# Kernel optimization log

Measured on AMD Instinct MI355X. Metric: run time of the kernel, lower is better.

## Reference

```python
import jax, jax.numpy as jnp
import numpy as np

B, S, H, V, MAXLEN = 32, 128, 512, 32000, 64


def setup_inputs() -> dict:
    key = jax.random.key(0)
    ks = jax.random.split(key, 10)
    s = 0.05
    return {
        "word_level_rep": jax.random.normal(ks[0], (B, S, H), jnp.float32),
        "sentence_level_rep": jax.random.normal(ks[1], (B, H), jnp.float32),
        "W2": jax.random.normal(ks[2], (H,), jnp.float32) * s,          # Linear(H,1,bias=False)
        "W4": jax.random.normal(ks[3], (H, 2 * H), jnp.float32) * s,    # Linear(2H,H,bias=False), torch layout [out,in]
        "W_ih": jax.random.normal(ks[4], (4 * H, H), jnp.float32) * s,  # LSTM gates i,f,g,o
        "W_hh": jax.random.normal(ks[5], (4 * H, H), jnp.float32) * s,
        "b_ih": jax.random.normal(ks[6], (4 * H,), jnp.float32) * s,
        "b_hh": jax.random.normal(ks[7], (4 * H,), jnp.float32) * s,
        "W_out": jax.random.normal(ks[8], (V, H), jnp.float32) * s,
        "b_out": jax.random.normal(ks[9], (V,), jnp.float32) * s,
        "max_len": MAXLEN,
    }


def reference(word_level_rep, sentence_level_rep, W2, W4, W_ih, W_hh, b_ih, b_hh, W_out, b_out, max_len):
    b, seq, h_dim = word_level_rep.shape

    def step(carry, _):
        h, c = carry
        # sentence-level attention over a singleton memory bank -> weight == 1
        sent_ctx = sentence_level_rep                                   # [B,H]
        # word-level Bahdanau attention
        scores = jnp.tanh(word_level_rep + h[:, None, :]) @ W2          # [B,S]
        attn = jax.nn.softmax(scores, axis=1)                           # [B,S]
        word_ctx = jnp.einsum('bs,bsh->bh', attn, word_level_rep)       # [B,H]
        x = jnp.tanh(jnp.concatenate([sent_ctx, word_ctx], axis=-1) @ W4.T)  # [B,H]
        # PyTorch LSTM cell: gates order i, f, g, o
        gates = x @ W_ih.T + b_ih + h @ W_hh.T + b_hh                   # [B,4H]
        i, f, g, o = jnp.split(gates, 4, axis=-1)
        c_new = jax.nn.sigmoid(f) * c + jax.nn.sigmoid(i) * jnp.tanh(g)
        h_new = jax.nn.sigmoid(o) * jnp.tanh(c_new)
        out = h_new @ W_out.T + b_out                                   # [B,V]
        return (h_new, c_new), out

    h0 = jnp.zeros((b, h_dim), word_level_rep.dtype)
    c0 = jnp.zeros((b, h_dim), word_level_rep.dtype)
    (h_fin, _), outs = jax.lax.scan(step, (h0, c0), None, length=max_len)
    generated_sequence = jnp.transpose(outs, (1, 0, 2))                 # [B,max_len,V]
    return generated_sequence, h_fin
```

## Files before the change

kernel.cpp:

```cpp
#include <hip/hip_runtime.h>
#include <stdint.h>

typedef unsigned short ushort_t;
typedef unsigned long long ull_t;
typedef __attribute__((ext_vector_type(8))) short bf16x8;
typedef __attribute__((ext_vector_type(8))) unsigned short u16x8;
typedef __attribute__((ext_vector_type(4))) unsigned short u16x4;
typedef __attribute__((ext_vector_type(4))) float f32x4;
typedef __attribute__((ext_vector_type(4))) unsigned u32x4;

#define DEV static __device__ __forceinline__
#define SCOPE_AGENT __HIP_MEMORY_SCOPE_AGENT

DEV unsigned short f2bf(float f) {
  unsigned u = __float_as_uint(f);
  u += 0x7FFFu + ((u >> 16) & 1u);
  return (unsigned short)(u >> 16);
}
DEV float bf2f(unsigned short h) { return __uint_as_float(((unsigned)h) << 16); }
DEV float fast_rcp(float x) { return __builtin_amdgcn_rcpf(x); }
DEV float fast_tanh(float x) { float e = __expf(2.f * x); return (e - 1.f) * fast_rcp(e + 1.f); }
DEV float fast_sigm(float x) { return fast_rcp(1.f + __expf(-x)); }

DEV float wave_sum(float v) {
#pragma unroll
  for (int d = 32; d > 0; d >>= 1) v += __shfl_xor(v, d, 64);
  return v;
}
DEV float wave_max(float v) {
#pragma unroll
  for (int d = 32; d > 0; d >>= 1) v = fmaxf(v, __shfl_xor(v, d, 64));
  return v;
}

DEV void async_g2l(const void* g, void* l) {
  __builtin_amdgcn_global_load_lds((const __attribute__((address_space(1))) void*)g,
                                   (__attribute__((address_space(3))) void*)l, 16, 0, 0);
}

DEV unsigned ld_flag(unsigned* p) { return __hip_atomic_load(p, __ATOMIC_RELAXED, SCOPE_AGENT); }
DEV void st_flag(unsigned* p, unsigned v) { __hip_atomic_store(p, v, __ATOMIC_RELAXED, SCOPE_AGENT); }
DEV void st_u64(ull_t* p, ull_t v) { __hip_atomic_store(p, v, __ATOMIC_RELAXED, SCOPE_AGENT); }
DEV void release_fence() { __builtin_amdgcn_s_waitcnt(0); }

DEV u32x4 ld_coh16(const void* p) {
  u32x4 v;
  asm volatile("global_load_dwordx4 %0, %1, off sc0 sc1" : "=v"(v) : "v"(p));
  return v;
}
DEV void wait_vm0() { asm volatile("s_waitcnt vmcnt(0)" ::: "memory"); }

__global__ __launch_bounds__(256) void k_initP(
    const float* __restrict__ w, const float* __restrict__ sent,
    const float* __restrict__ W4, ushort_t* __restrict__ P, float* __restrict__ sp)
{
  __shared__ float As2[16 * 68];
  __shared__ float Bs2[16 * 68];
  const int tid = threadIdx.x;
  const int m0 = blockIdx.x * 64, n0 = blockIdx.y * 64;
  const int tm = tid & 15, tn = tid >> 4;
  const bool sent_half = (m0 >= 4096);
  float acc[4][4];
#pragma unroll
  for (int i = 0; i < 4; i++)
#pragma unroll
    for (int j = 0; j < 4; j++) acc[i][j] = 0.f;

  for (int k0 = 0; k0 < 512; k0 += 16) {
#pragma unroll
    for (int i = 0; i < 4; i++) {
      int idx = i * 256 + tid;
      int r = idx >> 4, kk = idx & 15;
      int m = m0 + r;
      float va = 0.f;
      if (m < 4096) va = w[(size_t)m * 512 + k0 + kk];
      else if (m < 4128) va = sent[(m - 4096) * 512 + k0 + kk];
      As2[kk * 68 + r] = va;
      Bs2[kk * 68 + r] = W4[(size_t)(n0 + r) * 1024 + (sent_half ? 0 : 512) + k0 + kk];
    }
    __syncthreads();
#pragma unroll
    for (int k = 0; k < 16; k++) {
      f32x4 av = *(const f32x4*)&As2[k * 68 + tm * 4];
      f32x4 bv = *(const f32x4*)&Bs2[k * 68 + tn * 4];
#pragma unroll
      for (int i = 0; i < 4; i++)
#pragma unroll
        for (int j = 0; j < 4; j++) acc[i][j] = fmaf(av[i], bv[j], acc[i][j]);
    }
    __syncthreads();
  }
#pragma unroll
  for (int i = 0; i < 4; i++) {
    int m = m0 + tm * 4 + i;
    if (m >= 4128) continue;
#pragma unroll
    for (int j = 0; j < 4; j++) {
      int n = n0 + tn * 4 + j;
      if (m < 4096) P[(size_t)m * 512 + n] = f2bf(acc[i][j]);
      else sp[(m - 4096) * 512 + n] = acc[i][j];
    }
  }
}

struct GateS {
  ushort_t XH[32 * 520];
  float gates[32 * 132];
  float bias[128];
  float cstate[1024];
  ushort_t hs16[1024];
};
struct AttnS {
  float hs[512];
  float sps[512];
  float sc[128];
  float attw[128];
  float xpart[8 * 520];
  ushort_t xs16[512];
};

__global__ __launch_bounds__(512, 2) void k_recur(
    const float* __restrict__ W2, const float* __restrict__ W_ih, const float* __restrict__ W_hh,
    const float* __restrict__ b_ih, const float* __restrict__ b_hh,
    const float* __restrict__ word, const ushort_t* __restrict__ P, const float* __restrict__ sp,
    unsigned* hflag, unsigned* xflag, ull_t* hbuf, ull_t* xbuf,
    ull_t* __restrict__ h_A, float* __restrict__ h_fin,
    const float* __restrict__ W_out, ushort_t* __restrict__ Wout_bf)
{
  __shared__ union { GateS g; AttnS a; } sm;
  const int bid = blockIdx.x, tid = threadIdx.x;
  const int wv = tid >> 6, lane = tid & 63;

  if (bid >= 48) {
    int idx = (bid - 48) * 512 + tid;
    const int stp = (256 - 48) * 512;
    for (; idx < 4096000; idx += stp) {
      f32x4 v = *(const f32x4*)(W_out + (size_t)idx * 4);
      u16x4 o;
      o[0] = f2bf(v[0]); o[1] = f2bf(v[1]); o[2] = f2bf(v[2]); o[3] = f2bf(v[3]);
      *(u16x4*)(Wout_bf + (size_t)idx * 4) = o;
    }
    return;
  }

  if (bid < 16) {
    const int ln = lane & 15, quad = lane >> 4;
    const int grow = (wv >> 1) * 512 + (bid << 5) + ((wv & 1) << 4) + ln;
    sm.g.cstate[tid] = 0.f;
    sm.g.cstate[tid + 512] = 0.f;
    if (tid < 128) {
      int gr = (tid >> 5) * 512 + (bid << 5) + (tid & 31);
      sm.g.bias[tid] = b_ih[gr] + b_hh[gr];
    }
    bf16x8 fih[16], fhh[16];
#pragma unroll
    for (int ks = 0; ks < 16; ks++) {
      const float* pi = W_ih + (size_t)grow * 512 + ks * 32 + quad * 8;
      const float* ph = W_hh + (size_t)grow * 512 + ks * 32 + quad * 8;
#pragma unroll
      for (int j = 0; j < 8; j++) {
        fih[ks][j] = (short)f2bf(pi[j]);
        fhh[ks][j] = (short)f2bf(ph[j]);
      }
    }
    __syncthreads();

#define STAGE_XH(SRC)                                                         \
    {                                                                         \
      const char* src_ = (const char*)(SRC);                                  \
      u32x4 r0 = ld_coh16(src_ + (tid << 4));                                 \
      u32x4 r1 = ld_coh16(src_ + ((512 + tid) << 4));                         \
      u32x4 r2 = ld_coh16(src_ + ((1024 + tid) << 4));                        \
      u32x4 r3 = ld_coh16(src_ + ((1536 + tid) << 4));                        \
      wait_vm0();                                                             \
      int c1 = 512 + tid, c2 = 1024 + tid, c3 = 1536 + tid;                   \
      *(u32x4*)&sm.g.XH[(tid >> 6) * 520 + (tid & 63) * 8] = r0;              \
      *(u32x4*)&sm.g.XH[(c1 >> 6) * 520 + (c1 & 63) * 8] = r1;                \
      *(u32x4*)&sm.g.XH[(c2 >> 6) * 520 + (c2 & 63) * 8] = r2;                \
      *(u32x4*)&sm.g.XH[(c3 >> 6) * 520 + (c3 & 63) * 8] = r3;                \
    }

#define GATE_MFMA(FW)                                                         \
    _Pragma("unroll")                                                         \
    for (int ks = 0; ks < 16; ks++) {                                         \
      bf16x8 a0 = *(const bf16x8*)&sm.g.XH[ln * 520 + ks * 32 + quad * 8];    \
      bf16x8 a1 = *(const bf16x8*)&sm.g.XH[(16 + ln) * 520 + ks * 32 + quad * 8]; \
      acc0 = __builtin_amdgcn_mfma_f32_16x16x32_bf16(a0, FW[ks], acc0, 0, 0, 0);  \
      acc1 = __builtin_amdgcn_mfma_f32_16x16x32_bf16(a1, FW[ks], acc1, 0, 0, 0);  \
    }

    for (int t = 0; t < 64; t++) {
      if (t > 0 && tid < 16) {
        while (ld_flag(&hflag[tid]) < (unsigned)t) __builtin_amdgcn_s_sleep(1);
      }
      __syncthreads();
      STAGE_XH(hbuf + ((t + 1) & 1) * 4096);
      __syncthreads();
      f32x4 acc0 = {0.f, 0.f, 0.f, 0.f}, acc1 = {0.f, 0.f, 0.f, 0.f};
      GATE_MFMA(fhh)
      if (tid < 32) {
        while (ld_flag(&xflag[tid]) < (unsigned)(t + 1)) __builtin_amdgcn_s_sleep(1);
      }
      __syncthreads();
      STAGE_XH(xbuf);
      __syncthreads();
      GATE_MFMA(fih)
      {
        float bb = sm.g.bias[wv * 16 + ln];
#pragma unroll
        for (int reg = 0; reg < 4; reg++) {
          sm.g.gates[(quad * 4 + reg) * 132 + wv * 16 + ln] = acc0[reg] + bb;
          sm.g.gates[(16 + quad * 4 + reg) * 132 + wv * 16 + ln] = acc1[reg] + bb;
        }
      }
      __syncthreads();
#pragma unroll
      for (int i = 0; i < 2; i++) {
        int e = i * 512 + tid;
        int b = e >> 5, hd = e & 31;
        float gi = sm.g.gates[b * 132 + hd];
        float gf = sm.g.gates[b * 132 + 32 + hd];
        float gg = sm.g.gates[b * 132 + 64 + hd];
        float go = sm.g.gates[b * 132 + 96 + hd];
        float cold = sm.g.cstate[e];
        float cn = fast_sigm(gf) * cold + fast_sigm(gi) * fast_tanh(gg);
        float hn = fast_sigm(go) * fast_tanh(cn);
        sm.g.cstate[e] = cn;
        sm.g.hs16[e] = f2bf(hn);
        if (t == 63) h_fin[b * 512 + (bid << 5) + hd] = hn;
      }
      __syncthreads();
      if (tid < 256) {
        int b = tid >> 3, j = tid & 7;
        ull_t v = *(const ull_t*)&sm.g.hs16[(b << 5) + (j << 2)];
        st_u64(&hbuf[(t & 1) * 4096 + (b << 7) + (bid << 3) + j], v);
        h_A[(size_t)((b << 6) + t) * 128 + (bid << 3) + j] = v;
        release_fence();
      }
      __syncthreads();
      if (tid == 0) st_flag(&hflag[bid], (unsigned)(t + 1));
    }
#undef STAGE_XH
#undef GATE_MFMA
  } else {
    const int b = bid - 16;
    float w2v[8];
#pragma unroll
    for (int j = 0; j < 8; j++) w2v[j] = W2[lane * 8 + j];
    sm.a.sps[tid] = sp[b * 512 + tid];
    __syncthreads();

    for (int t = 0; t < 64; t++) {
      if (t > 0 && tid < 16) {
        while (ld_flag(&hflag[tid]) < (unsigned)t) __builtin_amdgcn_s_sleep(1);
      }
      __syncthreads();
      if (tid < 64) {
        u32x4 hv = ld_coh16((const char*)(hbuf + ((t + 1) & 1) * 4096) + b * 1024 + (tid << 4));
        wait_vm0();
#pragma unroll
        for (int j = 0; j < 4; j++) {
          sm.a.hs[tid * 8 + 2 * j]     = bf2f((ushort_t)(hv[j] & 0xffffu));
          sm.a.hs[tid * 8 + 2 * j + 1] = bf2f((ushort_t)(hv[j] >> 16));
        }
      }
      __syncthreads();
      float hf[8];
#pragma unroll
      for (int j = 0; j < 8; j++) hf[j] = sm.a.hs[lane * 8 + j];
      const float* wbase = word + (((size_t)b * 128 + wv * 16) << 9) + lane * 8;
#pragma unroll 2
      for (int i = 0; i < 16; i++) {
        const float* wp = wbase + ((size_t)i << 9);
        f32x4 wa = *(const f32x4*)wp;
        f32x4 wb = *(const f32x4*)(wp + 4);
        float acc = 0.f;
#pragma unroll
        for (int j = 0; j < 4; j++) {
          float v = wa[j] + hf[j];
          float e = __expf(v + v);
          acc = fmaf((e - 1.f) * fast_rcp(e + 1.f), w2v[j], acc);
        }
#pragma unroll
        for (int j = 0; j < 4; j++) {
          float v = wb[j] + hf[4 + j];
          float e = __expf(v + v);
          acc = fmaf((e - 1.f) * fast_rcp(e + 1.f), w2v[4 + j], acc);
        }
        acc = wave_sum(acc);
        if (lane == 0) sm.a.sc[wv * 16 + i] = acc;
      }
      __syncthreads();
      if (wv == 0) {
        float a0 = sm.a.sc[lane], a1 = sm.a.sc[lane + 64];
        float m = wave_max(fmaxf(a0, a1));
        float e0 = __expf(a0 - m), e1 = __expf(a1 - m);
        float inv = fast_rcp(wave_sum(e0 + e1));
        sm.a.attw[lane] = e0 * inv;
        sm.a.attw[lane + 64] = e1 * inv;
      }
      __syncthreads();
      {
        f32x4 xacc0 = {0.f, 0.f, 0.f, 0.f}, xacc1 = {0.f, 0.f, 0.f, 0.f};
        const ushort_t* Pb = P + (((size_t)b * 128 + wv * 16) << 9) + lane * 8;
#pragma unroll 4
        for (int i = 0; i < 16; i++) {
          float aw = sm.a.attw[wv * 16 + i];
          u16x8 pv = *(const u16x8*)(Pb + ((size_t)i << 9));
#pragma unroll
          for (int j = 0; j < 4; j++) xacc0[j] = fmaf(aw, bf2f(pv[j]), xacc0[j]);
#pragma unroll
          for (int j = 0; j < 4; j++) xacc1[j] = fmaf(aw, bf2f(pv[4 + j]), xacc1[j]);
        }
        *(f32x4*)&sm.a.xpart[wv * 520 + lane * 8] = xacc0;
        *(f32x4*)&sm.a.xpart[wv * 520 + lane * 8 + 4] = xacc1;
      }
      __syncthreads();
      {
        float xv = sm.a.sps[tid];
#pragma unroll
        for (int g = 0; g < 8; g++) xv += sm.a.xpart[g * 520 + tid];
        sm.a.xs16[tid] = f2bf(fast_tanh(xv));
      }
      __syncthreads();
      if (tid < 128) {
        ull_t v = *(const ull_t*)&sm.a.xs16[tid << 2];
        st_u64(&xbuf[(b << 7) + tid], v);
        release_fence();
      }
      __syncthreads();
      if (tid == 0) st_flag(&xflag[b], (unsigned)(t + 1));
    }
  }
}

__global__ __launch_bounds__(256) void k_gemm(
    const ushort_t* __restrict__ A, const ushort_t* __restrict__ Bw,
    const float* __restrict__ bias, float* __restrict__ C)
{
  __shared__ ushort_t As[128 * 64];
  __shared__ ushort_t Bs[128 * 64];
  const int tid = threadIdx.x;
  const int wave = tid >> 6, lane = tid & 63;
  const int ln = lane & 15, quad = lane >> 4;
  const int bm = blockIdx.x & 15, bn = blockIdx.x >> 4;
  const int wm = wave & 1, wn = wave >> 1;

  f32x4 acc[4][4];
#pragma unroll
  for (int i = 0; i < 4; i++)
#pragma unroll
    for (int j = 0; j < 4; j++) { acc[i][j][0] = 0.f; acc[i][j][1] = 0.f; acc[i][j][2] = 0.f; acc[i][j][3] = 0.f; }

  for (int kt = 0; kt < 8; kt++) {
    const int k0 = kt * 64;
#pragma unroll
    for (int i = 0; i < 4; i++) {
      int s = i * 256 + tid;
      int r = s >> 3, c = s & 7;
      int cs = c ^ (r & 7);
      async_g2l(A + ((size_t)(bm * 128 + r) << 9) + k0 + (cs << 3), &As[s << 3]);
    }
#pragma unroll
    for (int i = 0; i < 4; i++) {
      int s = i * 256 + tid;
      int r = s >> 3, c = s & 7;
      int cs = c ^ (r & 7);
      async_g2l(Bw + ((size_t)(bn * 128 + r) << 9) + k0 + (cs << 3), &Bs[s << 3]);
    }
    __syncthreads();
#pragma unroll
    for (int ks = 0; ks < 2; ks++) {
      bf16x8 af[4], bfr[4];
      int cc = ks * 4 + quad;
#pragma unroll
      for (int f = 0; f < 4; f++) {
        int ra = wm * 64 + f * 16 + ln;
        af[f] = *(const bf16x8*)&As[((ra << 3) + (cc ^ (ra & 7))) << 3];
        int rb = wn * 64 + f * 16 + ln;
        bfr[f] = *(const bf16x8*)&Bs[((rb << 3) + (cc ^ (rb & 7))) << 3];
      }
#pragma unroll
      for (int mf = 0; mf < 4; mf++)
#pragma unroll
        for (int nf = 0; nf < 4; nf++)
          acc[mf][nf] = __builtin_amdgcn_mfma_f32_16x16x32_bf16(af[mf], bfr[nf], acc[mf][nf], 0, 0, 0);
    }
    __syncthreads();
  }
#pragma unroll
  for (int nf = 0; nf < 4; nf++) {
    int n = bn * 128 + wn * 64 + nf * 16 + ln;
    float bv = bias[n];
#pragma unroll
    for (int mf = 0; mf < 4; mf++) {
      int mbase = bm * 128 + wm * 64 + mf * 16 + (quad << 2);
#pragma unroll
      for (int r = 0; r < 4; r++)
        C[(size_t)(mbase + r) * 32000 + n] = acc[mf][nf][r] + bv;
    }
  }
}

extern "C" void kernel_launch(void* const* d_in, const int* in_sizes, int n_in,
                              void* d_out, int out_size, void* d_ws, size_t ws_size,
                              hipStream_t stream) {
  const float* word  = (const float*)d_in[0];
  const float* sent  = (const float*)d_in[1];
  const float* W2    = (const float*)d_in[2];
  const float* W4    = (const float*)d_in[3];
  const float* W_ih  = (const float*)d_in[4];
  const float* W_hh  = (const float*)d_in[5];
  const float* b_ih  = (const float*)d_in[6];
  const float* b_hh  = (const float*)d_in[7];
  const float* W_out = (const float*)d_in[8];
  const float* b_out = (const float*)d_in[9];
  float* out = (float*)d_out;

  char* ws = (char*)d_ws;
  unsigned* hflag   = (unsigned*)(ws + 0);
  unsigned* xflag   = (unsigned*)(ws + 512);
  ull_t*    hbuf    = (ull_t*)(ws + 1024);
  ull_t*    xbuf    = (ull_t*)(ws + 66560);
  float*    sp      = (float*)(ws + 99328);
  ushort_t* P       = (ushort_t*)(ws + 164864);
  ull_t*    h_A     = (ull_t*)(ws + 8553472);
  ushort_t* Wout_bf = (ushort_t*)(ws + 10650624);
  float* h_fin = out + 65536000;

  hipMemsetAsync(ws, 0, 66560, stream);

  k_initP<<<dim3(65, 8), 256, 0, stream>>>(word, sent, W4, P, sp);
  k_recur<<<256, 512, 0, stream>>>(W2, W_ih, W_hh, b_ih, b_hh, word, P, sp,
                                   hflag, xflag, hbuf, xbuf, h_A, h_fin, W_out, Wout_bf);
  k_gemm<<<4000, 256, 0, stream>>>((const ushort_t*)h_A, Wout_bf, b_out, out);
}
```

Baseline: 1.778 ms.

## Convert word reps to bf16 and use whole-wave coherent flag polling

Adds a pre-pass that converts word_level_rep to bf16 in workspace, so the attention blocks read half the bytes per step for the tanh scoring. Flag waits change from per-thread relaxed atomic loads to a whole-wave poll with coherent loads and __all, sleeping longer between polls. The launch_bounds minimum-blocks hint is also dropped. The bf16 word values reduce precision in the attention scores, and the extra kernel adds a small launch cost.

```diff
diff --git a/kernel.cpp b/kernel.cpp
--- a/kernel.cpp
+++ b/kernel.cpp
@@ -48,7 +48,23 @@
   asm volatile("global_load_dwordx4 %0, %1, off sc0 sc1" : "=v"(v) : "v"(p));
   return v;
 }
+DEV unsigned ld_coh4(const unsigned* p) {
+  unsigned v;
+  asm volatile("global_load_dword %0, %1, off sc0 sc1" : "=v"(v) : "v"(p));
+  return v;
+}
 DEV void wait_vm0() { asm volatile("s_waitcnt vmcnt(0)" ::: "memory"); }
+
+__global__ void k_f2bf(const float* __restrict__ in, ushort_t* __restrict__ out, int n4) {
+  int i = blockIdx.x * blockDim.x + threadIdx.x;
+  int st = gridDim.x * blockDim.x;
+  for (; i < n4; i += st) {
+    f32x4 v = *(const f32x4*)(in + (size_t)i * 4);
+    u16x4 o;
+    o[0] = f2bf(v[0]); o[1] = f2bf(v[1]); o[2] = f2bf(v[2]); o[3] = f2bf(v[3]);
+    *(u16x4*)(out + (size_t)i * 4) = o;
+  }
+}
 
 __global__ __launch_bounds__(256) void k_initP(
     const float* __restrict__ w, const float* __restrict__ sent,
@@ -119,10 +135,10 @@
   ushort_t xs16[512];
 };
 
-__global__ __launch_bounds__(512, 2) void k_recur(
+__global__ __launch_bounds__(512) void k_recur(
     const float* __restrict__ W2, const float* __restrict__ W_ih, const float* __restrict__ W_hh,
     const float* __restrict__ b_ih, const float* __restrict__ b_hh,
-    const float* __restrict__ word, const ushort_t* __restrict__ P, const float* __restrict__ sp,
+    const ushort_t* __restrict__ w_bf, const ushort_t* __restrict__ P, const float* __restrict__ sp,
     unsigned* hflag, unsigned* xflag, ull_t* hbuf, ull_t* xbuf,
     ull_t* __restrict__ h_A, float* __restrict__ h_fin,
     const float* __restrict__ W_out, ushort_t* __restrict__ Wout_bf)
@@ -142,6 +158,21 @@
     }
     return;
   }
+
+#define POLL16(FLAGS, TVAL)                                               \
+    for (;;) {                                                            \
+      unsigned fv_ = ld_coh4(&(FLAGS)[lane & 15]);                        \
+      wait_vm0();                                                         \
+      if (__all((int)(fv_ >= (unsigned)(TVAL)))) break;                   \
+      __builtin_amdgcn_s_sleep(4);                                        \
+    }
+#define POLL32(FLAGS, TVAL)                                               \
+    for (;;) {                                                            \
+      unsigned fv_ = ld_coh4(&(FLAGS)[lane & 31]);                        \
+      wait_vm0();                                                         \
+      if (__all((int)(fv_ >= (unsigned)(TVAL)))) break;                   \
+      __builtin_amdgcn_s_sleep(4);                                        \
+    }
 
   if (bid < 16) {
     const int ln = lane & 15, quad = lane >> 4;
@@ -190,17 +221,13 @@
     }
 
     for (int t = 0; t < 64; t++) {
-      if (t > 0 && tid < 16) {
-        while (ld_flag(&hflag[tid]) < (unsigned)t) __builtin_amdgcn_s_sleep(1);
-      }
+      if (t > 0 && wv == 0) { POLL16(hflag, t) }
       __syncthreads();
       STAGE_XH(hbuf + ((t + 1) & 1) * 4096);
       __syncthreads();
       f32x4 acc0 = {0.f, 0.f, 0.f, 0.f}, acc1 = {0.f, 0.f, 0.f, 0.f};
       GATE_MFMA(fhh)
-      if (tid < 32) {
-        while (ld_flag(&xflag[tid]) < (unsigned)(t + 1)) __builtin_amdgcn_s_sleep(1);
-      }
+      if (wv == 0) { POLL32(xflag, t + 1) }
       __syncthreads();
       STAGE_XH(xbuf);
       __syncthreads();
@@ -231,10 +258,10 @@
       }
       __syncthreads();
       if (tid < 256) {
-        int b = tid >> 3, j = tid & 7;
-        ull_t v = *(const ull_t*)&sm.g.hs16[(b << 5) + (j << 2)];
-        st_u64(&hbuf[(t & 1) * 4096 + (b << 7) + (bid << 3) + j], v);
-        h_A[(size_t)((b << 6) + t) * 128 + (bid << 3) + j] = v;
+        int bb = tid >> 3, j = tid & 7;
+        ull_t v = *(const ull_t*)&sm.g.hs16[(bb << 5) + (j << 2)];
+        st_u64(&hbuf[(t & 1) * 4096 + (bb << 7) + (bid << 3) + j], v);
+        h_A[(size_t)((bb << 6) + t) * 128 + (bid << 3) + j] = v;
         release_fence();
       }
       __syncthreads();
@@ -251,12 +278,10 @@
     __syncthreads();
 
     for (int t = 0; t < 64; t++) {
-      if (t > 0 && tid < 16) {
-        while (ld_flag(&hflag[tid]) < (unsigned)t) __builtin_amdgcn_s_sleep(1);
-      }
+      if (t > 0 && wv == 0) { POLL16(hflag, t) }
       __syncthreads();
       if (tid < 64) {
-        u32x4 hv = ld_coh16((const char*)(hbuf + ((t + 1) & 1) * 4096) + b * 1024 + (tid << 4));
+        u32x4 hv = ld_coh16((const char*)hbuf + (((t + 1) & 1) << 15) + (b << 10) + (tid << 4));
         wait_vm0();
 #pragma unroll
         for (int j = 0; j < 4; j++) {
@@ -268,27 +293,19 @@
       float hf[8];
 #pragma unroll
       for (int j = 0; j < 8; j++) hf[j] = sm.a.hs[lane * 8 + j];
-      const float* wbase = word + (((size_t)b * 128 + wv * 16) << 9) + lane * 8;
 #pragma unroll 2
       for (int i = 0; i < 16; i++) {
-        const float* wp = wbase + ((size_t)i << 9);
-        f32x4 wa = *(const f32x4*)wp;
-        f32x4 wb = *(const f32x4*)(wp + 4);
+        int s = (wv << 4) + i;
+        u16x8 wvv = *(const u16x8*)(w_bf + ((size_t)((b << 7) + s) << 9) + (lane << 3));
         float acc = 0.f;
 #pragma unroll
-        for (int j = 0; j < 4; j++) {
-          float v = wa[j] + hf[j];
+        for (int j = 0; j < 8; j++) {
+          float v = bf2f(wvv[j]) + hf[j];
           float e = __expf(v + v);
           acc = fmaf((e - 1.f) * fast_rcp(e + 1.f), w2v[j], acc);
         }
-#pragma unroll
-        for (int j = 0; j < 4; j++) {
-          float v = wb[j] + hf[4 + j];
-          float e = __expf(v + v);
-          acc = fmaf((e - 1.f) * fast_rcp(e + 1.f), w2v[4 + j], acc);
-        }
         acc = wave_sum(acc);
-        if (lane == 0) sm.a.sc[wv * 16 + i] = acc;
+        if (lane == 0) sm.a.sc[s] = acc;
       }
       __syncthreads();
       if (wv == 0) {
@@ -302,10 +319,10 @@
       __syncthreads();
       {
         f32x4 xacc0 = {0.f, 0.f, 0.f, 0.f}, xacc1 = {0.f, 0.f, 0.f, 0.f};
-        const ushort_t* Pb = P + (((size_t)b * 128 + wv * 16) << 9) + lane * 8;
+        const ushort_t* Pb = P + (((size_t)b * 128 + (wv << 4)) << 9) + lane * 8;
 #pragma unroll 4
         for (int i = 0; i < 16; i++) {
-          float aw = sm.a.attw[wv * 16 + i];
+          float aw = sm.a.attw[(wv << 4) + i];
           u16x8 pv = *(const u16x8*)(Pb + ((size_t)i << 9));
 #pragma unroll
           for (int j = 0; j < 4; j++) xacc0[j] = fmaf(aw, bf2f(pv[j]), xacc0[j]);
@@ -332,6 +349,8 @@
       if (tid == 0) st_flag(&xflag[b], (unsigned)(t + 1));
     }
   }
+#undef POLL16
+#undef POLL32
 }
 
 __global__ __launch_bounds__(256) void k_gemm(
@@ -424,14 +443,16 @@
   ull_t*    xbuf    = (ull_t*)(ws + 66560);
   float*    sp      = (float*)(ws + 99328);
   ushort_t* P       = (ushort_t*)(ws + 164864);
+  ushort_t* w_bf    = (ushort_t*)(ws + 4359168);
   ull_t*    h_A     = (ull_t*)(ws + 8553472);
   ushort_t* Wout_bf = (ushort_t*)(ws + 10650624);
   float* h_fin = out + 65536000;
 
   hipMemsetAsync(ws, 0, 66560, stream);
 
+  k_f2bf<<<512, 256, 0, stream>>>(word, w_bf, 2097152 / 4);
   k_initP<<<dim3(65, 8), 256, 0, stream>>>(word, sent, W4, P, sp);
-  k_recur<<<256, 512, 0, stream>>>(W2, W_ih, W_hh, b_ih, b_hh, word, P, sp,
+  k_recur<<<256, 512, 0, stream>>>(W2, W_ih, W_hh, b_ih, b_hh, w_bf, P, sp,
                                    hflag, xflag, hbuf, xbuf, h_A, h_fin, W_out, Wout_bf);
   k_gemm<<<4000, 256, 0, stream>>>((const ushort_t*)h_A, Wout_bf, b_out, out);
 }
```

New measurement: 1.804 ms. No clear change (+1.5%).
